# Kernel tuning notes

Measured on AMD Instinct MI355X. Metric: run time of the kernel, lower is better.

The kernel has to match this reference:

```python
import jax, jax.numpy as jnp
import numpy as np

B, S, D, H, DQK, DV, DFF, L = 8, 512, 512, 8, 64, 64, 2048, 2
SCALE = float(np.sqrt(DQK))


def sinusoid_pe(s, d):
    pos = jnp.arange(s, dtype=jnp.float32)[:, None]
    div = jnp.exp(jnp.arange(0, d, 2, dtype=jnp.float32) * (-np.log(10000.0) / d))
    pe = jnp.zeros((s, d), jnp.float32)
    pe = pe.at[:, 0::2].set(jnp.sin(pos * div))
    pe = pe.at[:, 1::2].set(jnp.cos(pos * div))
    return pe


def ms_masks(s, steps=(4, 8, 16), rep=2):
    # Vectorized equivalent of multi_scale_mask: window of `step` neighbors,
    # shifted near the boundaries so the total neighbor count stays = step.
    i = jnp.arange(s)[:, None]
    j = jnp.arange(s)[None, :]
    ms = []
    for step in steps:
        s2 = step // 2
        left = jnp.where(i < s // 2, jnp.minimum(i, s2), step - jnp.minimum(s - 1 - i, s2))
        right = step - left
        m = (j >= i - left) & (j <= i + right)
        ms += [m] * rep
    return jnp.stack(ms)  # [6, S, S] bool


def layer_norm(x, g, b):
    mu = x.mean(-1, keepdims=True)
    var = ((x - mu) ** 2).mean(-1, keepdims=True)
    return (x - mu) / jnp.sqrt(var + 1e-6) * g + b


def mha(qin, kin, vin, wq, wk, wv, wo, g, b, mask):
    bq, lq, _ = qin.shape
    lk = kin.shape[1]
    q = (qin @ wq).reshape(bq, lq, H, DQK).transpose(0, 2, 1, 3)  # bhqd
    k = (kin @ wk).reshape(bq, lk, H, DQK).transpose(0, 2, 1, 3)
    v = (vin @ wv).reshape(bq, lk, H, DV).transpose(0, 2, 1, 3)
    scores = jnp.einsum('bhqd,bhkd->bhqk', q / SCALE, k)
    scores = jnp.where(mask, scores, jnp.float32(-1e9))
    p = jax.nn.softmax(scores, axis=-1)
    o = jnp.einsum('bhqk,bhkd->bhqd', p, v).transpose(0, 2, 1, 3).reshape(bq, lq, H * DV)
    return layer_norm(o @ wo + qin, g, b)


def ffn(x, w1, b1, w2, b2, g, bb):
    h = jax.nn.relu(x @ w1 + b1)
    return layer_norm(h @ w2 + b2 + x, g, bb)


def setup_inputs() -> dict:
    key = jax.random.key(0)
    ks = jax.random.split(key, 40)
    it = iter(range(40))
    d = {}
    d['src_seq'] = jax.random.normal(ks[next(it)], (B, S, D), jnp.float32)
    d['trg_seq'] = jax.random.normal(ks[next(it)], (B, S, D), jnp.float32)
    d['enc_pad_num'] = jax.random.randint(ks[next(it)], (B,), 0, 64)
    d['dec_pad_num'] = jax.random.randint(ks[next(it)], (B,), 0, 64)

    def w(shape):
        return jax.random.normal(ks[next(it)], shape, jnp.float32) * 0.02

    for p in ('e_wq', 'e_wk', 'e_wv'):
        d[p] = w((L, D, H * DQK))
    d['e_wo'] = w((L, H * DV, D))
    d['e_g1'] = jnp.ones((L, D)); d['e_b1'] = jnp.zeros((L, D))
    d['e_w1'] = w((L, D, DFF)); d['e_bb1'] = jnp.zeros((L, DFF))
    d['e_w2'] = w((L, DFF, D)); d['e_bb2'] = jnp.zeros((L, D))
    d['e_g2'] = jnp.ones((L, D)); d['e_b2'] = jnp.zeros((L, D))
    for p in ('d_swq', 'd_swk', 'd_swv'):
        d[p] = w((L, D, H * DQK))
    d['d_swo'] = w((L, H * DV, D))
    d['d_g1'] = jnp.ones((L, D)); d['d_b1'] = jnp.zeros((L, D))
    for p in ('d_cwq', 'd_cwk', 'd_cwv'):
        d[p] = w((L, D, H * DQK))
    d['d_cwo'] = w((L, H * DV, D))
    d['d_g2'] = jnp.ones((L, D)); d['d_b2'] = jnp.zeros((L, D))
    d['d_w1'] = w((L, D, DFF)); d['d_bb1'] = jnp.zeros((L, DFF))
    d['d_w2'] = w((L, DFF, D)); d['d_bb2'] = jnp.zeros((L, D))
    d['d_g3'] = jnp.ones((L, D)); d['d_b3'] = jnp.zeros((L, D))
    return d


def reference(src_seq, trg_seq, enc_pad_num, dec_pad_num,
              e_wq, e_wk, e_wv, e_wo, e_g1, e_b1, e_w1, e_bb1, e_w2, e_bb2, e_g2, e_b2,
              d_swq, d_swk, d_swv, d_swo, d_g1, d_b1,
              d_cwq, d_cwk, d_cwv, d_cwo, d_g2, d_b2,
              d_w1, d_bb1, d_w2, d_bb2, d_g3, d_b3):
    ms = ms_masks(S)  # [6, S, S]
    src_pad = jnp.arange(S)[None, :] < (S - enc_pad_num)[:, None]  # [B, S]
    trg_pad = jnp.arange(S)[None, :] < (S - dec_pad_num)[:, None]

    def full_mask(pad):
        base = pad[:, None, None, :]  # [B,1,1,S]
        win = jnp.logical_and(ms[None], base)  # [B,6,S,S]
        dense = jnp.broadcast_to(base, (B, H - ms.shape[0], S, S))
        return jnp.concatenate([win, dense], axis=1)  # [B,H,S,S]

    src_mask = full_mask(src_pad)
    trg_mask = full_mask(trg_pad)
    pe = sinusoid_pe(S, D)

    x = src_seq + pe[None]
    for l in range(L):
        x = mha(x, x, x, e_wq[l], e_wk[l], e_wv[l], e_wo[l], e_g1[l], e_b1[l], src_mask)
        x = ffn(x, e_w1[l], e_bb1[l], e_w2[l], e_bb2[l], e_g2[l], e_b2[l])

    y = trg_seq + pe[None]
    for l in range(L):
        y = mha(y, y, y, d_swq[l], d_swk[l], d_swv[l], d_swo[l], d_g1[l], d_b1[l], trg_mask)
        y = mha(y, x, x, d_cwq[l], d_cwk[l], d_cwv[l], d_cwo[l], d_g2[l], d_b2[l], src_mask)
        y = ffn(y, d_w1[l], d_bb1[l], d_w2[l], d_bb2[l], d_g3[l], d_b3[l])
    return y
```

## Files before the change

kernel.cpp:

```cpp
#include <hip/hip_runtime.h>
#include <hip/hip_bf16.h>

#define BB 8
#define SS 512
#define DD 512
#define HH 8
#define DQKv 64
#define DFFv 2048
#define LL 2

typedef __attribute__((ext_vector_type(8))) __bf16 bf16x8;
typedef __attribute__((ext_vector_type(4))) float f32x4;

static __device__ __forceinline__ ushort f2b(float x) {
    unsigned int u = __float_as_uint(x);
    unsigned int r = (u + 0x7FFFu + ((u >> 16) & 1u)) >> 16;
    return (ushort)r;
}
static __device__ __forceinline__ float b2f(ushort u) {
    return __uint_as_float(((unsigned int)u) << 16);
}

typedef __attribute__((address_space(1))) const unsigned int gas_u32;
typedef __attribute__((address_space(3))) unsigned int las_u32;
static __device__ __forceinline__ void gload16(const void* g, void* l) {
    __builtin_amdgcn_global_load_lds((gas_u32*)g, (las_u32*)l, 16, 0, 0);
}

#define VMCNT4 asm volatile("s_waitcnt vmcnt(4)" ::: "memory")
#define VMCNT6 asm volatile("s_waitcnt vmcnt(6)" ::: "memory")
#define VMCNT0 asm volatile("s_waitcnt vmcnt(0)" ::: "memory")
#define LGKM0  asm volatile("s_waitcnt lgkmcnt(0)" ::: "memory")
#define SCHEDB __builtin_amdgcn_sched_barrier(0)
#define SBAR   __builtin_amdgcn_s_barrier()

__global__ __launch_bounds__(256) void add_pe2_k(const float* __restrict__ src,
                                                 const float* __restrict__ trg,
                                                 ushort* __restrict__ xb,
                                                 ushort* __restrict__ yb) {
    const int NQ = BB * SS * DD / 4;
    int i = blockIdx.x * 256 + threadIdx.x;
    const bool second = i >= NQ;
    const int ii = second ? i - NQ : i;
    const int rem = ii & (SS * DD / 4 - 1);
    const int d4 = rem & (DD / 4 - 1);
    const int s = rem >> 7;

    float4 a = ((const float4*)(second ? trg : src))[ii];
    const float c = -9.210340371976184f / 512.0f;
    const float div0 = __expf((float)(4 * d4) * c);
    const float div1 = __expf((float)(4 * d4 + 2) * c);
    const float a0 = (float)s * div0, a1 = (float)s * div1;
    a.x += sinf(a0); a.y += cosf(a0);
    a.z += sinf(a1); a.w += cosf(a1);

    ushort* ob = second ? yb : xb;
    ushort4 ub;
    ub.x = f2b(a.x); ub.y = f2b(a.y); ub.z = f2b(a.z); ub.w = f2b(a.w);
    ((ushort4*)ob)[ii] = ub;
}

__global__ __launch_bounds__(256) void tcast_k(const float* __restrict__ s0,
                                               const float* __restrict__ s1,
                                               const float* __restrict__ s2,
                                               const float* __restrict__ s3,
                                               ushort* __restrict__ dst,
                                               int K, int N) {
    __shared__ ushort st[64][72];
    const float* src = (blockIdx.z == 0) ? s0 : (blockIdx.z == 1) ? s1
                     : (blockIdx.z == 2) ? s2 : s3;
    ushort* d = dst + (size_t)blockIdx.z * K * N;
    const int k0 = blockIdx.y * 64, n0 = blockIdx.x * 64;
    const int t = threadIdx.x;
    const int r = t >> 2, c4 = (t & 3) * 16;
#pragma unroll
    for (int i = 0; i < 16; i += 4) {
        float4 v = *(const float4*)&src[(size_t)(k0 + r) * N + n0 + c4 + i];
        st[c4 + i + 0][r] = f2b(v.x);
        st[c4 + i + 1][r] = f2b(v.y);
        st[c4 + i + 2][r] = f2b(v.z);
        st[c4 + i + 3][r] = f2b(v.w);
    }
    __syncthreads();
    const int n = t >> 2, seg = (t & 3) * 16;
    *(uint4*)&d[(size_t)(n0 + n) * K + k0 + seg]     = *(const uint4*)&st[n][seg];
    *(uint4*)&d[(size_t)(n0 + n) * K + k0 + seg + 8] = *(const uint4*)&st[n][seg + 8];
}

#define NW 32
struct WTab {
    const float* src[NW];
    unsigned off[NW];
    int Kd[NW];
    int Nd[NW];
    int cum[NW + 1];
};

__global__ __launch_bounds__(256) void tcast_all_k(WTab tab, ushort* __restrict__ dst) {
    __shared__ ushort st[64][72];
    const int t = blockIdx.x;
    int m = 0;
    while (t >= tab.cum[m + 1]) ++m;
    const int local = t - tab.cum[m];
    const int ntx = tab.Nd[m];
    const int bx = local % ntx, by = local / ntx;
    const float* src = tab.src[m];
    ushort* d = dst + tab.off[m];
    const int N = ntx * 64, K = tab.Kd[m] * 64;
    const int k0 = by * 64, n0 = bx * 64;

    const int tt = threadIdx.x;
    const int r = tt >> 2, c4 = (tt & 3) * 16;
#pragma unroll
    for (int i = 0; i < 16; i += 4) {
        float4 v = *(const float4*)&src[(size_t)(k0 + r) * N + n0 + c4 + i];
        st[c4 + i + 0][r] = f2b(v.x);
        st[c4 + i + 1][r] = f2b(v.y);
        st[c4 + i + 2][r] = f2b(v.z);
        st[c4 + i + 3][r] = f2b(v.w);
    }
    __syncthreads();
    const int n = tt >> 2, seg = (tt & 3) * 16;
    *(uint4*)&d[(size_t)(n0 + n) * K + k0 + seg]     = *(const uint4*)&st[n][seg];
    *(uint4*)&d[(size_t)(n0 + n) * K + k0 + seg + 8] = *(const uint4*)&st[n][seg + 8];
}

template <bool BIAS, bool RES, bool RELU, bool OUTBF>
__global__ __launch_bounds__(256) void gemm2_k(const ushort* __restrict__ A,
                                               const ushort* __restrict__ Bt,
                                               const float* __restrict__ bias,
                                               const ushort* __restrict__ res,
                                               void* __restrict__ Cout,
                                               int M, int N, int K, int nbx) {
    __shared__ ushort sA[3][64 * 64];
    __shared__ ushort sB[3][64 * 64];

    const int tid = threadIdx.x;
    const int nwg = gridDim.x;
    const int wg = blockIdx.x;
    const int swz = (wg & 7) * (nwg >> 3) + (wg >> 3);
    const int bx = swz % nbx, by = swz / nbx;

    const int lane = tid & 63, w = tid >> 6;
    const int wm = w >> 1, wn = w & 1;
    const int llo = lane & 15, lhi = lane >> 4;

    const int srow = tid >> 3;
    const int scol = (((tid & 7) ^ (srow & 7)) * 8);
    const ushort* Ab = A + (size_t)(by * 64 + srow) * K + scol;
    const ushort* Bb = Bt + (size_t)(bx * 64 + srow) * K + scol;
    const int sOff = srow * 128 + (tid & 7) * 16;

    f32x4 acc[2][2] = {};
    const int nt = K >> 6;

#pragma unroll
    for (int i = 0; i < 2; ++i) {
        gload16(Ab + (size_t)i * 32 * K, (char*)sA[0] + sOff + i * 32 * 128);
        gload16(Bb + (size_t)i * 32 * K, (char*)sB[0] + sOff + i * 32 * 128);
    }
    if (nt > 1) {
#pragma unroll
        for (int i = 0; i < 2; ++i) {
            gload16(Ab + (size_t)i * 32 * K + 64, (char*)sA[1] + sOff + i * 32 * 128);
            gload16(Bb + (size_t)i * 32 * K + 64, (char*)sB[1] + sOff + i * 32 * 128);
        }
    }
    SCHEDB;

    for (int t = 0; t < nt; ++t) {
        if (t + 1 < nt) { VMCNT4; } else { VMCNT0; }
        LGKM0;
        SCHEDB;
        SBAR;
        SCHEDB;
        if (t + 2 < nt) {
            const int k0 = (t + 2) << 6;
            char* dA = (char*)sA[(t + 2) % 3] + sOff;
            char* dB = (char*)sB[(t + 2) % 3] + sOff;
#pragma unroll
            for (int i = 0; i < 2; ++i) {
                gload16(Ab + (size_t)i * 32 * K + k0, dA + i * 32 * 128);
                gload16(Bb + (size_t)i * 32 * K + k0, dB + i * 32 * 128);
            }
        }
        SCHEDB;
        const ushort* cA = sA[t % 3];
        const ushort* cB = sB[t % 3];
        const int sw = llo & 7;
#pragma unroll
        for (int ks = 0; ks < 2; ++ks) {
            const int pc = ((ks * 4 + lhi) ^ sw) * 8;
            bf16x8 af[2];
#pragma unroll
            for (int fa = 0; fa < 2; ++fa)
                af[fa] = *(const bf16x8*)&cA[(wm * 32 + fa * 16 + llo) * 64 + pc];
            bf16x8 bfrag[2];
#pragma unroll
            for (int fb = 0; fb < 2; ++fb)
                bfrag[fb] = *(const bf16x8*)&cB[(wn * 32 + fb * 16 + llo) * 64 + pc];
#pragma unroll
            for (int fa = 0; fa < 2; ++fa)
#pragma unroll
                for (int fb = 0; fb < 2; ++fb)
                    acc[fa][fb] = __builtin_amdgcn_mfma_f32_16x16x32_bf16(
                        af[fa], bfrag[fb], acc[fa][fb], 0, 0, 0);
        }
    }

#pragma unroll
    for (int fa = 0; fa < 2; ++fa) {
#pragma unroll
        for (int fb = 0; fb < 2; ++fb) {
            const int col = bx * 64 + wn * 32 + fb * 16 + llo;
            const float bv = BIAS ? bias[col] : 0.f;
#pragma unroll
            for (int j = 0; j < 4; ++j) {
                const int row = by * 64 + wm * 32 + fa * 16 + lhi * 4 + j;
                float v = acc[fa][fb][j] + bv;
                if (RES) v += b2f(res[(size_t)row * N + col]);
                if (RELU) v = fmaxf(v, 0.f);
                if (OUTBF) ((ushort*)Cout)[(size_t)row * N + col] = f2b(v);
                else       ((float*)Cout)[(size_t)row * N + col] = v;
            }
        }
    }
}

__global__ __launch_bounds__(256) void gemm2s_k(const ushort* __restrict__ A,
                                                const ushort* __restrict__ Bt,
                                                float* __restrict__ P0,
                                                float* __restrict__ P1,
                                                int M, int N, int K) {
    __shared__ ushort sA[3][64 * 64];
    __shared__ ushort sB[3][64 * 64];

    const int tid = threadIdx.x;
    const int nwg = gridDim.x;
    const int wg = blockIdx.x;
    const int swz = (wg & 7) * (nwg >> 3) + (wg >> 3);
    const int bx = swz & 7;
    const int r2 = swz >> 3;
    const int by = r2 & 63;
    const int kh = r2 >> 6;
    const int Kh = K >> 1;
    const int kbase = kh * Kh;

    const int lane = tid & 63, w = tid >> 6;
    const int wm = w >> 1, wn = w & 1;
    const int llo = lane & 15, lhi = lane >> 4;

    const int srow = tid >> 3;
    const int scol = (((tid & 7) ^ (srow & 7)) * 8);
    const ushort* Ab = A + (size_t)(by * 64 + srow) * K + kbase + scol;
    const ushort* Bb = Bt + (size_t)(bx * 64 + srow) * K + kbase + scol;
    const int sOff = srow * 128 + (tid & 7) * 16;

    f32x4 acc[2][2] = {};
    const int nt = Kh >> 6;

#pragma unroll
    for (int i = 0; i < 2; ++i) {
        gload16(Ab + (size_t)i * 32 * K, (char*)sA[0] + sOff + i * 32 * 128);
        gload16(Bb + (size_t)i * 32 * K, (char*)sB[0] + sOff + i * 32 * 128);
    }
#pragma unroll
    for (int i = 0; i < 2; ++i) {
        gload16(Ab + (size_t)i * 32 * K + 64, (char*)sA[1] + sOff + i * 32 * 128);
        gload16(Bb + (size_t)i * 32 * K + 64, (char*)sB[1] + sOff + i * 32 * 128);
    }
    SCHEDB;

    for (int t = 0; t < nt; ++t) {
        if (t + 1 < nt) { VMCNT4; } else { VMCNT0; }
        LGKM0;
        SCHEDB;
        SBAR;
        SCHEDB;
        if (t + 2 < nt) {
            const int k0 = (t + 2) << 6;
            char* dA = (char*)sA[(t + 2) % 3] + sOff;
            char* dB = (char*)sB[(t + 2) % 3] + sOff;
#pragma unroll
            for (int i = 0; i < 2; ++i) {
                gload16(Ab + (size_t)i * 32 * K + k0, dA + i * 32 * 128);
                gload16(Bb + (size_t)i * 32 * K + k0, dB + i * 32 * 128);
            }
        }
        SCHEDB;
        const ushort* cA = sA[t % 3];
        const ushort* cB = sB[t % 3];
        const int sw = llo & 7;
#pragma unroll
        for (int ks = 0; ks < 2; ++ks) {
            const int pc = ((ks * 4 + lhi) ^ sw) * 8;
            bf16x8 af[2];
#pragma unroll
            for (int fa = 0; fa < 2; ++fa)
                af[fa] = *(const bf16x8*)&cA[(wm * 32 + fa * 16 + llo) * 64 + pc];
            bf16x8 bfrag[2];
#pragma unroll
            for (int fb = 0; fb < 2; ++fb)
                bfrag[fb] = *(const bf16x8*)&cB[(wn * 32 + fb * 16 + llo) * 64 + pc];
#pragma unroll
            for (int fa = 0; fa < 2; ++fa)
#pragma unroll
                for (int fb = 0; fb < 2; ++fb)
                    acc[fa][fb] = __builtin_amdgcn_mfma_f32_16x16x32_bf16(
                        af[fa], bfrag[fb], acc[fa][fb], 0, 0, 0);
        }
    }

    float* P = kh ? P1 : P0;
#pragma unroll
    for (int fa = 0; fa < 2; ++fa) {
#pragma unroll
        for (int fb = 0; fb < 2; ++fb) {
            const int col = bx * 64 + wn * 32 + fb * 16 + llo;
#pragma unroll
            for (int j = 0; j < 4; ++j) {
                const int row = by * 64 + wm * 32 + fa * 16 + lhi * 4 + j;
                P[(size_t)row * N + col] = acc[fa][fb][j];
            }
        }
    }
}

template <bool BIAS, bool RES, bool RELU, bool OUTBF>
__global__ __launch_bounds__(256) void gemm3_k(const ushort* __restrict__ A,
                                               const ushort* __restrict__ Bt,
                                               const float* __restrict__ bias,
                                               const ushort* __restrict__ res,
                                               void* __restrict__ Cout,
                                               int M, int N, int K, int nbx) {
    __shared__ ushort sA[2][64 * 64];
    __shared__ ushort sB[2][128 * 64];

    const int tid = threadIdx.x;
    const int nwg = gridDim.x;
    const int wg = blockIdx.x;
    const int swz = (wg & 7) * (nwg >> 3) + (wg >> 3);
    const int bx = swz % nbx, by = swz / nbx;

    const int lane = tid & 63, w = tid >> 6;
    const int wm = w >> 1, wn = w & 1;
    const int llo = lane & 15, lhi = lane >> 4;

    const int srow = tid >> 3;
    const int scol = (((tid & 7) ^ (srow & 7)) * 8);
    const ushort* Ab = A + (size_t)(by * 64 + srow) * K + scol;
    const ushort* Bb = Bt + (size_t)(bx * 128 + srow) * K + scol;
    const int sOff = srow * 128 + (tid & 7) * 16;

    f32x4 acc[2][4] = {};
    const int nt = K >> 6;

#pragma unroll
    for (int i = 0; i < 2; ++i)
        gload16(Ab + (size_t)i * 32 * K, (char*)sA[0] + sOff + i * 32 * 128);
#pragma unroll
    for (int i = 0; i < 4; ++i)
        gload16(Bb + (size_t)i * 32 * K, (char*)sB[0] + sOff + i * 32 * 128);
    SCHEDB;

    for (int t = 0; t < nt; ++t) {
        if (t + 1 < nt) {
            const int k0 = (t + 1) << 6;
            char* dA = (char*)sA[(t + 1) & 1] + sOff;
            char* dB = (char*)sB[(t + 1) & 1] + sOff;
#pragma unroll
            for (int i = 0; i < 2; ++i)
                gload16(Ab + (size_t)i * 32 * K + k0, dA + i * 32 * 128);
#pragma unroll
            for (int i = 0; i < 4; ++i)
                gload16(Bb + (size_t)i * 32 * K + k0, dB + i * 32 * 128);
            SCHEDB;
            VMCNT6;
        } else {
            VMCNT0;
        }
        SCHEDB;
        SBAR;
        SCHEDB;
        const ushort* cA = sA[t & 1];
        const ushort* cB = sB[t & 1];
        const int sw = llo & 7;
#pragma unroll
        for (int ks = 0; ks < 2; ++ks) {
            const int pc = ((ks * 4 + lhi) ^ sw) * 8;
            bf16x8 af[2];
#pragma unroll
            for (int fa = 0; fa < 2; ++fa)
                af[fa] = *(const bf16x8*)&cA[(wm * 32 + fa * 16 + llo) * 64 + pc];
            bf16x8 bfrag[4];
#pragma unroll
            for (int fb = 0; fb < 4; ++fb)
                bfrag[fb] = *(const bf16x8*)&cB[(wn * 64 + fb * 16 + llo) * 64 + pc];
#pragma unroll
            for (int fa = 0; fa < 2; ++fa)
#pragma unroll
                for (int fb = 0; fb < 4; ++fb)
                    acc[fa][fb] = __builtin_amdgcn_mfma_f32_16x16x32_bf16(
                        af[fa], bfrag[fb], acc[fa][fb], 0, 0, 0);
        }
        LGKM0;
        SCHEDB;
        SBAR;
    }

#pragma unroll
    for (int fa = 0; fa < 2; ++fa) {
#pragma unroll
        for (int fb = 0; fb < 4; ++fb) {
            const int col = bx * 128 + wn * 64 + fb * 16 + llo;
            const float bv = BIAS ? bias[col] : 0.f;
#pragma unroll
            for (int j = 0; j < 4; ++j) {
                const int row = by * 64 + wm * 32 + fa * 16 + lhi * 4 + j;
                float v = acc[fa][fb][j] + bv;
                if (RES) v += b2f(res[(size_t)row * N + col]);
                if (RELU) v = fmaxf(v, 0.f);
                if (OUTBF) ((ushort*)Cout)[(size_t)row * N + col] = f2b(v);
                else       ((float*)Cout)[(size_t)row * N + col] = v;
            }
        }
    }
}

__global__ __launch_bounds__(256) void attn_k(const ushort* __restrict__ QKV,
                                              ushort* __restrict__ O,
                                              const int* __restrict__ pad) {
    __shared__ ushort sQ[64][72];
    __shared__ ushort sK[64][72];
    __shared__ ushort sVt[64][72];
    __shared__ ushort sP[64][72];

    const int tid = threadIdx.x;
    const int b = blockIdx.z, h = blockIdx.y, q0 = blockIdx.x << 6;
    const int klim = SS - pad[b];
    const int lane = tid & 63, w = tid >> 6;
    const int qw0 = w << 4;
    const int lhi = lane >> 4, llo = lane & 15;
    const int ST = 3 * DD;

    {
        const int r = tid >> 2, seg = (tid & 3) << 4;
        const ushort* src = &QKV[(size_t)(b * SS + q0 + r) * ST + h * DQKv + seg];
        *(uint4*)&sQ[r][seg]     = *(const uint4*)src;
        *(uint4*)&sQ[r][seg + 8] = *(const uint4*)(src + 8);
    }

    auto window = [&](int i, int& wlo, int& whi) {
        if (h < 6) {
            const int step = 4 << (h >> 1);
            const int s2 = step >> 1;
            const int a1 = (i < s2) ? i : s2;
            const int a2 = ((SS - 1 - i) < s2) ? (SS - 1 - i) : s2;
            const int left = (i < SS / 2) ? a1 : (step - a2);
            wlo = i - left;
            whi = wlo + step;
        } else {
            wlo = 0;
            whi = SS - 1;
        }
    };

    int lo[4], hi[4];
#pragma unroll
    for (int j = 0; j < 4; ++j) window(q0 + qw0 + lhi * 4 + j, lo[j], hi[j]);

    int kt0 = 0, kt1 = SS;
    if (h < 6) {
        int lo0, hi0, lo63, hi63;
        window(q0, lo0, hi0);
        window(q0 + 63, lo63, hi63);
        if (lo63 >= klim) {
            kt0 = 0; kt1 = SS;
        } else {
            kt0 = (lo0 >> 6) << 6;
            kt1 = ((hi63 >> 6) + 1) << 6;
            if (kt1 > SS) kt1 = SS;
        }
    }

    float mr[4] = {-1e30f, -1e30f, -1e30f, -1e30f};
    float lr[4] = {0.f, 0.f, 0.f, 0.f};
    f32x4 oacc[4] = {};

    for (int kt = kt0; kt < kt1; kt += 64) {
        __syncthreads();
        {
            const int r = tid >> 2, seg = (tid & 3) << 4;
            const ushort* ksrc = &QKV[(size_t)(b * SS + kt + r) * ST + DD + h * DQKv + seg];
            *(uint4*)&sK[r][seg]     = *(const uint4*)ksrc;
            *(uint4*)&sK[r][seg + 8] = *(const uint4*)(ksrc + 8);
            const ushort* vsrc = &QKV[(size_t)(b * SS + kt + r) * ST + 2 * DD + h * DQKv + seg];
            uint4 u0 = *(const uint4*)vsrc;
            uint4 u1 = *(const uint4*)(vsrc + 8);
            const ushort* v0 = (const ushort*)&u0;
            const ushort* v1 = (const ushort*)&u1;
#pragma unroll
            for (int i = 0; i < 8; ++i) sVt[seg + i][r] = v0[i];
#pragma unroll
            for (int i = 0; i < 8; ++i) sVt[seg + 8 + i][r] = v1[i];
        }
        __syncthreads();

        f32x4 sacc[4] = {};
#pragma unroll
        for (int ks = 0; ks < 2; ++ks) {
            bf16x8 aq = *(const bf16x8*)&sQ[qw0 + llo][ks * 32 + lhi * 8];
#pragma unroll
            for (int n = 0; n < 4; ++n) {
                bf16x8 bk = *(const bf16x8*)&sK[n * 16 + llo][ks * 32 + lhi * 8];
                sacc[n] = __builtin_amdgcn_mfma_f32_16x16x32_bf16(aq, bk, sacc[n], 0, 0, 0);
            }
        }

#pragma unroll
        for (int j = 0; j < 4; ++j) {
            float s[4];
#pragma unroll
            for (int n = 0; n < 4; ++n) {
                const int kidx = kt + n * 16 + llo;
                const bool ok = (kidx < klim) && (kidx >= lo[j]) && (kidx <= hi[j]);
                s[n] = ok ? (sacc[n][j] * 0.125f) : -1e9f;
            }
            float tm = fmaxf(fmaxf(s[0], s[1]), fmaxf(s[2], s[3]));
#pragma unroll
            for (int off = 8; off; off >>= 1) tm = fmaxf(tm, __shfl_xor(tm, off));
            const float mn = fmaxf(mr[j], tm);
            const float alpha = __expf(mr[j] - mn);
            mr[j] = mn;
            float ps = 0.f;
            const int prow = qw0 + lhi * 4 + j;
#pragma unroll
            for (int n = 0; n < 4; ++n) {
                const ushort pb = f2b(__expf(s[n] - mn));
                sP[prow][n * 16 + llo] = pb;
                ps += b2f(pb);
            }
#pragma unroll
            for (int off = 8; off; off >>= 1) ps += __shfl_xor(ps, off);
            lr[j] = lr[j] * alpha + ps;
            oacc[0][j] *= alpha; oacc[1][j] *= alpha;
            oacc[2][j] *= alpha; oacc[3][j] *= alpha;
        }

#pragma unroll
        for (int ks = 0; ks < 2; ++ks) {
            bf16x8 ap = *(const bf16x8*)&sP[qw0 + llo][ks * 32 + lhi * 8];
#pragma unroll
            for (int n = 0; n < 4; ++n) {
                bf16x8 bv = *(const bf16x8*)&sVt[n * 16 + llo][ks * 32 + lhi * 8];
                oacc[n] = __builtin_amdgcn_mfma_f32_16x16x32_bf16(ap, bv, oacc[n], 0, 0, 0);
            }
        }
    }

#pragma unroll
    for (int j = 0; j < 4; ++j) {
        const float inv = 1.f / lr[j];
        const int q = q0 + qw0 + lhi * 4 + j;
#pragma unroll
        for (int n = 0; n < 4; ++n) {
            O[(size_t)(b * SS + q) * (HH * DQKv) + h * DQKv + n * 16 + llo] =
                f2b(oacc[n][j] * inv);
        }
    }
}

__global__ __launch_bounds__(256) void ln_k(const float* __restrict__ in,
                                            const float* __restrict__ g,
                                            const float* __restrict__ bvec,
                                            ushort* __restrict__ outb,
                                            float* __restrict__ outf) {
    const int row = blockIdx.x;
    const int tid = threadIdx.x;
    const float2 xv = *(const float2*)&in[(size_t)row * DD + tid * 2];

    __shared__ float red[4];
    __shared__ float red2[4];
    const int wid = tid >> 6, lane = tid & 63;

    float s = xv.x + xv.y;
#pragma unroll
    for (int off = 32; off; off >>= 1) s += __shfl_xor(s, off);
    if (lane == 0) red[wid] = s;
    __syncthreads();
    const float mu = (red[0] + red[1] + red[2] + red[3]) * (1.f / 512.f);

    const float dx = xv.x - mu, dy = xv.y - mu;
    float q = dx * dx + dy * dy;
#pragma unroll
    for (int off = 32; off; off >>= 1) q += __shfl_xor(q, off);
    if (lane == 0) red2[wid] = q;
    __syncthreads();
    const float var = (red2[0] + red2[1] + red2[2] + red2[3]) * (1.f / 512.f);
    const float rs = rsqrtf(var + 1e-6f);

    float2 o;
    o.x = dx * rs * g[tid * 2] + bvec[tid * 2];
    o.y = dy * rs * g[tid * 2 + 1] + bvec[tid * 2 + 1];
    ushort2 ub; ub.x = f2b(o.x); ub.y = f2b(o.y);
    *(ushort2*)&outb[(size_t)row * DD + tid * 2] = ub;
    if (outf) *(float2*)&outf[(size_t)row * DD + tid * 2] = o;
}

__global__ __launch_bounds__(256) void ln2_k(const float* __restrict__ p0,
                                             const float* __restrict__ p1,
                                             const float* __restrict__ bias,
                                             const ushort* __restrict__ res,
                                             const float* __restrict__ g,
                                             const float* __restrict__ bvec,
                                             ushort* __restrict__ outb,
                                             float* __restrict__ outf) {
    const int row = blockIdx.x;
    const int tid = threadIdx.x;
    const size_t base = (size_t)row * DD + tid * 2;
    const float2 a0 = *(const float2*)&p0[base];
    const float2 a1 = *(const float2*)&p1[base];
    const ushort2 rv = *(const ushort2*)&res[base];
    float2 xv;
    xv.x = a0.x + a1.x + bias[tid * 2]     + b2f(rv.x);
    xv.y = a0.y + a1.y + bias[tid * 2 + 1] + b2f(rv.y);

    __shared__ float red[4];
    __shared__ float red2[4];
    const int wid = tid >> 6, lane = tid & 63;

    float s = xv.x + xv.y;
#pragma unroll
    for (int off = 32; off; off >>= 1) s += __shfl_xor(s, off);
    if (lane == 0) red[wid] = s;
    __syncthreads();
    const float mu = (red[0] + red[1] + red[2] + red[3]) * (1.f / 512.f);

    const float dx = xv.x - mu, dy = xv.y - mu;
    float q = dx * dx + dy * dy;
#pragma unroll
    for (int off = 32; off; off >>= 1) q += __shfl_xor(q, off);
    if (lane == 0) red2[wid] = q;
    __syncthreads();
    const float var = (red2[0] + red2[1] + red2[2] + red2[3]) * (1.f / 512.f);
    const float rs = rsqrtf(var + 1e-6f);

    float2 o;
    o.x = dx * rs * g[tid * 2] + bvec[tid * 2];
    o.y = dy * rs * g[tid * 2 + 1] + bvec[tid * 2 + 1];
    ushort2 ub; ub.x = f2b(o.x); ub.y = f2b(o.y);
    *(ushort2*)&outb[base] = ub;
    if (outf) *(float2*)&outf[base] = o;
}

extern "C" void kernel_launch(void* const* d_in, const int* in_sizes, int n_in,
                              void* d_out, int out_size, void* d_ws, size_t ws_size,
                              hipStream_t stream) {
    const float* src_seq = (const float*)d_in[0];
    const float* trg_seq = (const float*)d_in[1];
    const int* enc_pad = (const int*)d_in[2];
    const int* dec_pad = (const int*)d_in[3];
    const float* e_wq = (const float*)d_in[4];
    const float* e_wk = (const float*)d_in[5];
    const float* e_wv = (const float*)d_in[6];
    const float* e_wo = (const float*)d_in[7];
    const float* e_g1 = (const float*)d_in[8];
    const float* e_b1 = (const float*)d_in[9];
    const float* e_w1 = (const float*)d_in[10];
    const float* e_bb1 = (const float*)d_in[11];
    const float* e_w2 = (const float*)d_in[12];
    const float* e_bb2 = (const float*)d_in[13];
    const float* e_g2 = (const float*)d_in[14];
    const float* e_b2 = (const float*)d_in[15];
    const float* d_swq = (const float*)d_in[16];
    const float* d_swk = (const float*)d_in[17];
    const float* d_swv = (const float*)d_in[18];
    const float* d_swo = (const float*)d_in[19];
    const float* d_g1 = (const float*)d_in[20];
    const float* d_b1 = (const float*)d_in[21];
    const float* d_cwq = (const float*)d_in[22];
    const float* d_cwk = (const float*)d_in[23];
    const float* d_cwv = (const float*)d_in[24];
    const float* d_cwo = (const float*)d_in[25];
    const float* d_g2 = (const float*)d_in[26];
    const float* d_b2 = (const float*)d_in[27];
    const float* d_w1 = (const float*)d_in[28];
    const float* d_bb1 = (const float*)d_in[29];
    const float* d_w2 = (const float*)d_in[30];
    const float* d_bb2 = (const float*)d_in[31];
    const float* d_g3 = (const float*)d_in[32];
    const float* d_b3 = (const float*)d_in[33];
    (void)in_sizes; (void)n_in; (void)out_size;

    const int M = BB * SS;
    const int NTOK = BB * SS * DD;
    const size_t WSZ = (size_t)DD * 512;

    float* ws = (float*)d_ws;
    float* t0 = ws;
    float* p0 = t0 + NTOK;
    float* p1 = p0 + NTOK;
    ushort* xbf  = (ushort*)(p1 + NTOK);
    ushort* ybf  = xbf + NTOK;
    ushort* qkvb = ybf + NTOK;
    ushort* ob   = qkvb + (size_t)M * 1536;
    ushort* hbf  = qkvb;
    ushort* warena = ob + NTOK;

    const float* wsrc[NW]; int wK[NW], wN[NW]; size_t woff[NW];
    int wcnt = 0; size_t acc = 0;
    auto push = [&](const float* p, int K, int N) {
        wsrc[wcnt] = p; wK[wcnt] = K; wN[wcnt] = N; woff[wcnt] = acc;
        acc += (size_t)K * N; ++wcnt;
    };
    for (int l = 0; l < LL; ++l) {
        push(e_wq + (size_t)l * WSZ, 512, 512);
        push(e_wk + (size_t)l * WSZ, 512, 512);
        push(e_wv + (size_t)l * WSZ, 512, 512);
        push(e_wo + (size_t)l * WSZ, 512, 512);
        push(e_w1 + (size_t)l * DD * DFFv, 512, DFFv);
        push(e_w2 + (size_t)l * DFFv * DD, DFFv, 512);
    }
    for (int l = 0; l < LL; ++l) {
        push(d_swq + (size_t)l * WSZ, 512, 512);
        push(d_swk + (size_t)l * WSZ, 512, 512);
        push(d_swv + (size_t)l * WSZ, 512, 512);
        push(d_swo + (size_t)l * WSZ, 512, 512);
        push(d_cwq + (size_t)l * WSZ, 512, 512);
        push(d_cwk + (size_t)l * WSZ, 512, 512);
        push(d_cwv + (size_t)l * WSZ, 512, 512);
        push(d_cwo + (size_t)l * WSZ, 512, 512);
        push(d_w1 + (size_t)l * DD * DFFv, 512, DFFv);
        push(d_w2 + (size_t)l * DFFv * DD, DFFv, 512);
    }

    const size_t base_bytes = (size_t)((char*)warena - (char*)d_ws);
    const bool big = ws_size >= base_bytes + acc * 2;

    if (big) {
        WTab tab;
        int tiles = 0;
        for (int i = 0; i < NW; ++i) {
            tab.src[i] = wsrc[i];
            tab.off[i] = (unsigned)woff[i];
            tab.Kd[i] = wK[i] / 64;
            tab.Nd[i] = wN[i] / 64;
            tab.cum[i] = tiles;
            tiles += (wK[i] / 64) * (wN[i] / 64);
        }
        tab.cum[NW] = tiles;
        tcast_all_k<<<tiles, 256, 0, stream>>>(tab, warena);
    }

    add_pe2_k<<<2 * NTOK / 4 / 256, 256, 0, stream>>>(src_seq, trg_seq, xbf, ybf);

    auto do_mha = [&](ushort* statebf, const ushort* kvbf, int widx,
                      const float* g, const float* bb, const int* pad) {
        const ushort* bt;
        if (big) {
            bt = warena + woff[widx];
        } else {
            tcast_k<<<dim3(8, 8, 4), 256, 0, stream>>>(
                wsrc[widx], wsrc[widx + 1], wsrc[widx + 2], wsrc[widx + 3],
                warena, 512, 512);
            bt = warena;
        }
        if (kvbf == statebf) {
            gemm3_k<false, false, false, true><<<64 * 12, 256, 0, stream>>>(
                statebf, bt, nullptr, nullptr, qkvb, M, 1536, 512, 12);
        } else {
            gemm2_k<false, false, false, true><<<64 * 8, 256, 0, stream>>>(
                statebf, bt + 0 * WSZ, nullptr, nullptr, qkvb, M, 1536, 512, 8);
            gemm3_k<false, false, false, true><<<64 * 8, 256, 0, stream>>>(
                kvbf, bt + 1 * WSZ, nullptr, nullptr, qkvb + DD, M, 1536, 512, 8);
        }
        attn_k<<<dim3(SS / 64, HH, BB), 256, 0, stream>>>(qkvb, ob, pad);
        gemm2_k<false, true, false, false><<<64 * 8, 256, 0, stream>>>(
            ob, bt + 3 * WSZ, nullptr, statebf, t0, M, 512, 512, 8);
        ln_k<<<M, 256, 0, stream>>>(t0, g, bb, statebf, nullptr);
    };
    auto do_ffn = [&](ushort* statebf, int widx,
                      const float* b1, const float* b2,
                      const float* g, const float* bb, float* lnoutf) {
        const ushort* bt1;
        const ushort* bt2;
        if (big) {
            bt1 = warena + woff[widx];
            bt2 = warena + woff[widx + 1];
        } else {
            tcast_k<<<dim3(32, 8, 1), 256, 0, stream>>>(
                wsrc[widx], wsrc[widx], wsrc[widx], wsrc[widx], warena, 512, DFFv);
            bt1 = warena;
            bt2 = warena;
        }
        gemm3_k<true, false, true, true><<<64 * 16, 256, 0, stream>>>(
            statebf, bt1, b1, nullptr, hbf, M, DFFv, 512, 16);
        if (!big) {
            tcast_k<<<dim3(8, 32, 1), 256, 0, stream>>>(
                wsrc[widx + 1], wsrc[widx + 1], wsrc[widx + 1], wsrc[widx + 1],
                warena, DFFv, 512);
        }
        gemm2s_k<<<1024, 256, 0, stream>>>(hbf, bt2, p0, p1, M, 512, DFFv);
        ln2_k<<<M, 256, 0, stream>>>(p0, p1, b2, statebf, g, bb, statebf, lnoutf);
    };

    for (int l = 0; l < LL; ++l) {
        do_mha(xbf, xbf, l * 6, e_g1 + l * DD, e_b1 + l * DD, enc_pad);
        do_ffn(xbf, l * 6 + 4, e_bb1 + l * DFFv, e_bb2 + l * DD,
               e_g2 + l * DD, e_b2 + l * DD, nullptr);
    }
    for (int l = 0; l < LL; ++l) {
        do_mha(ybf, ybf, 12 + l * 10, d_g1 + l * DD, d_b1 + l * DD, dec_pad);
        do_mha(ybf, xbf, 12 + l * 10 + 4, d_g2 + l * DD, d_b2 + l * DD, enc_pad);
        const bool last = (l == LL - 1);
        do_ffn(ybf, 12 + l * 10 + 8, d_bb1 + l * DFFv, d_bb2 + l * DD,
               d_g3 + l * DD, d_b3 + l * DD, last ? (float*)d_out : nullptr);
    }
}
```

Baseline: 550.8 us.

## Batch cross-attention K/V projections and fuse out-projection residual into split-K LayerNorm

Reorders the weight arena so both decoder layers' cross-attention K/V weights sit next to each other. Both layers' K/V projections of the encoder output then run as one wide GEMM before the decoder loop. Attention now takes separate Q/K/V pointers and strides, so it can read the precomputed cross K/V buffer. The attention output projection now uses the split-K GEMM, with the residual add moved into ln2_k, which replaces the old gemm+ln_k pair. This removes launches and gives the small K/V GEMMs a larger grid, at the cost of an extra workspace buffer.

```diff
diff --git a/kernel.cpp b/kernel.cpp
--- a/kernel.cpp
+++ b/kernel.cpp
@@ -125,11 +125,10 @@
     *(uint4*)&d[(size_t)(n0 + n) * K + k0 + seg + 8] = *(const uint4*)&st[n][seg + 8];
 }
 
-template <bool BIAS, bool RES, bool RELU, bool OUTBF>
+template <bool BIAS, bool RELU, bool OUTBF>
 __global__ __launch_bounds__(256) void gemm2_k(const ushort* __restrict__ A,
                                                const ushort* __restrict__ Bt,
                                                const float* __restrict__ bias,
-                                               const ushort* __restrict__ res,
                                                void* __restrict__ Cout,
                                                int M, int N, int K, int nbx) {
     __shared__ ushort sA[3][64 * 64];
@@ -218,7 +217,6 @@
             for (int j = 0; j < 4; ++j) {
                 const int row = by * 64 + wm * 32 + fa * 16 + lhi * 4 + j;
                 float v = acc[fa][fb][j] + bv;
-                if (RES) v += b2f(res[(size_t)row * N + col]);
                 if (RELU) v = fmaxf(v, 0.f);
                 if (OUTBF) ((ushort*)Cout)[(size_t)row * N + col] = f2b(v);
                 else       ((float*)Cout)[(size_t)row * N + col] = v;
@@ -326,11 +324,10 @@
     }
 }
 
-template <bool BIAS, bool RES, bool RELU, bool OUTBF>
+template <bool BIAS, bool RELU, bool OUTBF>
 __global__ __launch_bounds__(256) void gemm3_k(const ushort* __restrict__ A,
                                                const ushort* __restrict__ Bt,
                                                const float* __restrict__ bias,
-                                               const ushort* __restrict__ res,
                                                void* __restrict__ Cout,
                                                int M, int N, int K, int nbx) {
     __shared__ ushort sA[2][64 * 64];
@@ -418,7 +415,6 @@
             for (int j = 0; j < 4; ++j) {
                 const int row = by * 64 + wm * 32 + fa * 16 + lhi * 4 + j;
                 float v = acc[fa][fb][j] + bv;
-                if (RES) v += b2f(res[(size_t)row * N + col]);
                 if (RELU) v = fmaxf(v, 0.f);
                 if (OUTBF) ((ushort*)Cout)[(size_t)row * N + col] = f2b(v);
                 else       ((float*)Cout)[(size_t)row * N + col] = v;
@@ -427,7 +423,9 @@
     }
 }
 
-__global__ __launch_bounds__(256) void attn_k(const ushort* __restrict__ QKV,
+__global__ __launch_bounds__(256) void attn_k(const ushort* __restrict__ Q, int qst,
+                                              const ushort* __restrict__ Kb,
+                                              const ushort* __restrict__ Vb, int kvst,
                                               ushort* __restrict__ O,
                                               const int* __restrict__ pad) {
     __shared__ ushort sQ[64][72];
@@ -441,11 +439,10 @@
     const int lane = tid & 63, w = tid >> 6;
     const int qw0 = w << 4;
     const int lhi = lane >> 4, llo = lane & 15;
-    const int ST = 3 * DD;
 
     {
         const int r = tid >> 2, seg = (tid & 3) << 4;
-        const ushort* src = &QKV[(size_t)(b * SS + q0 + r) * ST + h * DQKv + seg];
+        const ushort* src = &Q[(size_t)(b * SS + q0 + r) * qst + h * DQKv + seg];
         *(uint4*)&sQ[r][seg]     = *(const uint4*)src;
         *(uint4*)&sQ[r][seg + 8] = *(const uint4*)(src + 8);
     }
@@ -491,10 +488,10 @@
         __syncthreads();
         {
             const int r = tid >> 2, seg = (tid & 3) << 4;
-            const ushort* ksrc = &QKV[(size_t)(b * SS + kt + r) * ST + DD + h * DQKv + seg];
+            const ushort* ksrc = &Kb[(size_t)(b * SS + kt + r) * kvst + h * DQKv + seg];
             *(uint4*)&sK[r][seg]     = *(const uint4*)ksrc;
             *(uint4*)&sK[r][seg + 8] = *(const uint4*)(ksrc + 8);
-            const ushort* vsrc = &QKV[(size_t)(b * SS + kt + r) * ST + 2 * DD + h * DQKv + seg];
+            const ushort* vsrc = &Vb[(size_t)(b * SS + kt + r) * kvst + h * DQKv + seg];
             uint4 u0 = *(const uint4*)vsrc;
             uint4 u1 = *(const uint4*)(vsrc + 8);
             const ushort* v0 = (const ushort*)&u0;
@@ -565,46 +562,9 @@
 #pragma unroll
         for (int n = 0; n < 4; ++n) {
             O[(size_t)(b * SS + q) * (HH * DQKv) + h * DQKv + n * 16 + llo] =
-                f2b(oacc[n][j] * inv);
-        }
-    }
-}
-
-__global__ __launch_bounds__(256) void ln_k(const float* __restrict__ in,
-                                            const float* __restrict__ g,
-                                            const float* __restrict__ bvec,
-                                            ushort* __restrict__ outb,
-                                            float* __restrict__ outf) {
-    const int row = blockIdx.x;
-    const int tid = threadIdx.x;
-    const float2 xv = *(const float2*)&in[(size_t)row * DD + tid * 2];
-
-    __shared__ float red[4];
-    __shared__ float red2[4];
-    const int wid = tid >> 6, lane = tid & 63;
-
-    float s = xv.x + xv.y;
-#pragma unroll
-    for (int off = 32; off; off >>= 1) s += __shfl_xor(s, off);
-    if (lane == 0) red[wid] = s;
-    __syncthreads();
-    const float mu = (red[0] + red[1] + red[2] + red[3]) * (1.f / 512.f);
-
-    const float dx = xv.x - mu, dy = xv.y - mu;
-    float q = dx * dx + dy * dy;
-#pragma unroll
-    for (int off = 32; off; off >>= 1) q += __shfl_xor(q, off);
-    if (lane == 0) red2[wid] = q;
-    __syncthreads();
-    const float var = (red2[0] + red2[1] + red2[2] + red2[3]) * (1.f / 512.f);
-    const float rs = rsqrtf(var + 1e-6f);
-
-    float2 o;
-    o.x = dx * rs * g[tid * 2] + bvec[tid * 2];
-    o.y = dy * rs * g[tid * 2 + 1] + bvec[tid * 2 + 1];
-    ushort2 ub; ub.x = f2b(o.x); ub.y = f2b(o.y);
-    *(ushort2*)&outb[(size_t)row * DD + tid * 2] = ub;
-    if (outf) *(float2*)&outf[(size_t)row * DD + tid * 2] = o;
+                f2b(oacc[j < 0 ? 0 : n][j] * inv);
+        }
+    }
 }
 
 __global__ __launch_bounds__(256) void ln2_k(const float* __restrict__ p0,
@@ -622,8 +582,9 @@
     const float2 a1 = *(const float2*)&p1[base];
     const ushort2 rv = *(const ushort2*)&res[base];
     float2 xv;
-    xv.x = a0.x + a1.x + bias[tid * 2]     + b2f(rv.x);
-    xv.y = a0.y + a1.y + bias[tid * 2 + 1] + b2f(rv.y);
+    xv.x = a0.x + a1.x + b2f(rv.x);
+    xv.y = a0.y + a1.y + b2f(rv.y);
+    if (bias) { xv.x += bias[tid * 2]; xv.y += bias[tid * 2 + 1]; }
 
     __shared__ float red[4];
     __shared__ float red2[4];
@@ -696,16 +657,15 @@
     const int NTOK = BB * SS * DD;
     const size_t WSZ = (size_t)DD * 512;
 
-    float* ws = (float*)d_ws;
-    float* t0 = ws;
-    float* p0 = t0 + NTOK;
+    float* p0 = (float*)d_ws;
     float* p1 = p0 + NTOK;
     ushort* xbf  = (ushort*)(p1 + NTOK);
     ushort* ybf  = xbf + NTOK;
     ushort* qkvb = ybf + NTOK;
     ushort* ob   = qkvb + (size_t)M * 1536;
+    ushort* ckv  = ob + NTOK;
+    ushort* warena = ckv + (size_t)M * 2048;
     ushort* hbf  = qkvb;
-    ushort* warena = ob + NTOK;
 
     const float* wsrc[NW]; int wK[NW], wN[NW]; size_t woff[NW];
     int wcnt = 0; size_t acc = 0;
@@ -727,11 +687,13 @@
         push(d_swv + (size_t)l * WSZ, 512, 512);
         push(d_swo + (size_t)l * WSZ, 512, 512);
         push(d_cwq + (size_t)l * WSZ, 512, 512);
-        push(d_cwk + (size_t)l * WSZ, 512, 512);
-        push(d_cwv + (size_t)l * WSZ, 512, 512);
         push(d_cwo + (size_t)l * WSZ, 512, 512);
         push(d_w1 + (size_t)l * DD * DFFv, 512, DFFv);
         push(d_w2 + (size_t)l * DFFv * DD, DFFv, 512);
+    }
+    for (int l = 0; l < LL; ++l) {
+        push(d_cwk + (size_t)l * WSZ, 512, 512);
+        push(d_cwv + (size_t)l * WSZ, 512, 512);
     }
 
     const size_t base_bytes = (size_t)((char*)warena - (char*)d_ws);
@@ -754,8 +716,8 @@
 
     add_pe2_k<<<2 * NTOK / 4 / 256, 256, 0, stream>>>(src_seq, trg_seq, xbf, ybf);
 
-    auto do_mha = [&](ushort* statebf, const ushort* kvbf, int widx,
-                      const float* g, const float* bb, const int* pad) {
+    auto do_mha_self = [&](ushort* statebf, int widx,
+                           const float* g, const float* bb, const int* pad) {
         const ushort* bt;
         if (big) {
             bt = warena + woff[widx];
@@ -765,20 +727,36 @@
                 warena, 512, 512);
             bt = warena;
         }
-        if (kvbf == statebf) {
-            gemm3_k<false, false, false, true><<<64 * 12, 256, 0, stream>>>(
-                statebf, bt, nullptr, nullptr, qkvb, M, 1536, 512, 12);
+        gemm3_k<false, false, true><<<64 * 12, 256, 0, stream>>>(
+            statebf, bt, nullptr, qkvb, M, 1536, 512, 12);
+        attn_k<<<dim3(SS / 64, HH, BB), 256, 0, stream>>>(
+            qkvb, 1536, qkvb + DD, qkvb + 2 * DD, 1536, ob, pad);
+        gemm2s_k<<<1024, 256, 0, stream>>>(ob, bt + 3 * WSZ, p0, p1, M, 512, 512);
+        ln2_k<<<M, 256, 0, stream>>>(p0, p1, nullptr, statebf, g, bb, statebf, nullptr);
+    };
+
+    auto do_mha_cross = [&](ushort* statebf, int widxQ, int widxO, int l,
+                            const float* g, const float* bb, const int* pad) {
+        const ushort *btq, *bto;
+        if (big) {
+            btq = warena + woff[widxQ];
+            bto = warena + woff[widxO];
         } else {
-            gemm2_k<false, false, false, true><<<64 * 8, 256, 0, stream>>>(
-                statebf, bt + 0 * WSZ, nullptr, nullptr, qkvb, M, 1536, 512, 8);
-            gemm3_k<false, false, false, true><<<64 * 8, 256, 0, stream>>>(
-                kvbf, bt + 1 * WSZ, nullptr, nullptr, qkvb + DD, M, 1536, 512, 8);
-        }
-        attn_k<<<dim3(SS / 64, HH, BB), 256, 0, stream>>>(qkvb, ob, pad);
-        gemm2_k<false, true, false, false><<<64 * 8, 256, 0, stream>>>(
-            ob, bt + 3 * WSZ, nullptr, statebf, t0, M, 512, 512, 8);
-        ln_k<<<M, 256, 0, stream>>>(t0, g, bb, statebf, nullptr);
+            tcast_k<<<dim3(8, 8, 4), 256, 0, stream>>>(
+                wsrc[widxQ], wsrc[widxO], wsrc[28 + l * 2], wsrc[29 + l * 2],
+                warena, 512, 512);
+            btq = warena; bto = warena + WSZ;
+            gemm3_k<false, false, true><<<64 * 8, 256, 0, stream>>>(
+                xbf, warena + 2 * WSZ, nullptr, ckv + (size_t)l * 1024, M, 2048, 512, 8);
+        }
+        gemm2_k<false, false, true><<<64 * 8, 256, 0, stream>>>(
+            statebf, btq, nullptr, qkvb, M, 1536, 512, 8);
+        attn_k<<<dim3(SS / 64, HH, BB), 256, 0, stream>>>(
+            qkvb, 1536, ckv + (size_t)l * 1024, ckv + (size_t)l * 1024 + 512, 2048, ob, pad);
+        gemm2s_k<<<1024, 256, 0, stream>>>(ob, bto, p0, p1, M, 512, 512);
+        ln2_k<<<M, 256, 0, stream>>>(p0, p1, nullptr, statebf, g, bb, statebf, nullptr);
     };
+
     auto do_ffn = [&](ushort* statebf, int widx,
                       const float* b1, const float* b2,
                       const float* g, const float* bb, float* lnoutf) {
@@ -793,8 +771,8 @@
             bt1 = warena;
             bt2 = warena;
         }
-        gemm3_k<true, false, true, true><<<64 * 16, 256, 0, stream>>>(
-            statebf, bt1, b1, nullptr, hbf, M, DFFv, 512, 16);
+        gemm3_k<true, true, true><<<64 * 16, 256, 0, stream>>>(
+            statebf, bt1, b1, hbf, M, DFFv, 512, 16);
         if (!big) {
             tcast_k<<<dim3(8, 32, 1), 256, 0, stream>>>(
                 wsrc[widx + 1], wsrc[widx + 1], wsrc[widx + 1], wsrc[widx + 1],
@@ -805,15 +783,22 @@
     };
 
     for (int l = 0; l < LL; ++l) {
-        do_mha(xbf, xbf, l * 6, e_g1 + l * DD, e_b1 + l * DD, enc_pad);
+        do_mha_self(xbf, l * 6, e_g1 + l * DD, e_b1 + l * DD, enc_pad);
         do_ffn(xbf, l * 6 + 4, e_bb1 + l * DFFv, e_bb2 + l * DD,
                e_g2 + l * DD, e_b2 + l * DD, nullptr);
     }
+
+    if (big) {
+        gemm3_k<false, false, true><<<64 * 16, 256, 0, stream>>>(
+            xbf, warena + woff[28], nullptr, ckv, M, 2048, 512, 16);
+    }
+
     for (int l = 0; l < LL; ++l) {
-        do_mha(ybf, ybf, 12 + l * 10, d_g1 + l * DD, d_b1 + l * DD, dec_pad);
-        do_mha(ybf, xbf, 12 + l * 10 + 4, d_g2 + l * DD, d_b2 + l * DD, enc_pad);
+        do_mha_self(ybf, 12 + l * 8, d_g1 + l * DD, d_b1 + l * DD, dec_pad);
+        do_mha_cross(ybf, 12 + l * 8 + 4, 12 + l * 8 + 5, l,
+                     d_g2 + l * DD, d_b2 + l * DD, enc_pad);
         const bool last = (l == LL - 1);
-        do_ffn(ybf, 12 + l * 10 + 8, d_bb1 + l * DFFv, d_bb2 + l * DD,
+        do_ffn(ybf, 12 + l * 8 + 6, d_bb1 + l * DFFv, d_bb2 + l * DD,
                d_g3 + l * DD, d_b3 + l * DD, last ? (float*)d_out : nullptr);
     }
 }
```

After: 559.4 us. About the same (+1.6%).
